# Performance work log

Measured on AMD Instinct MI355X. Metric: run time of the kernel, lower is better.

## Reference

```python
import jax, jax.numpy as jnp
import numpy as np

IN_DIM, OUT_DIM = 64, 64
HIDDEN = [64, 64, 64]
D = IN_DIM * OUT_DIM  # number of independent per-edge small MLPs
B = 256


def setup_inputs() -> dict:
    key = jax.random.key(0)
    ks = jax.random.split(key, 10)

    def kaiming(k, shape, fan_in):
        # kaiming_uniform_ with a=0, nonlinearity='relu': bound = sqrt(6/fan_in)
        bound = np.sqrt(6.0 / fan_in)
        return jax.random.uniform(k, shape, jnp.float32, -bound, bound)

    def bias_init(k, shape, fan_in):
        bound = 1.0 / np.sqrt(fan_in)
        return jax.random.uniform(k, shape, jnp.float32, -bound, bound)

    h0, h1, h2 = HIDDEN
    inp = {
        "x": jax.random.normal(ks[0], (B, IN_DIM), jnp.float32),
        # Input_Linear: weight (out_dim, in_dim, h0); fan_in per torch kaiming on this tensor is in_dim*h0,
        # bias uses reset_parameters(1) -> fan_in=1
        "w0": kaiming(ks[1], (OUT_DIM, IN_DIM, h0), IN_DIM * h0),
        "b0": bias_init(ks[2], (D, h0), 1),
        # Linear(d, o=h1, i=h0): weight (d, h1, h0); kaiming fan_in = h0 (last dim), bias fan_in = i = h0
        "w1": kaiming(ks[3], (D, h1, h0), h0),
        "b1": bias_init(ks[4], (D, h1), h0),
        "w2": kaiming(ks[5], (D, h2, h1), h1),
        "b2": bias_init(ks[6], (D, h2), h1),
        # Output_Linear: weight (out_dim, in_dim*h2), fan_in = in_dim*h2
        "wout": kaiming(ks[7], (OUT_DIM, IN_DIM * h2), IN_DIM * h2),
        "bout": bias_init(ks[8], (OUT_DIM,), IN_DIM * h2),
    }
    return inp


def reference(x, w0, b0, w1, b1, w2, b2, wout, bout):
    Bsz = x.shape[0]
    # Input_Linear: broadcast outer product -> (B, out_dim, in_dim, h0) -> (B, d, h0)
    out = x[:, None, :, None] * w0[None, :, :, :]
    out = out.reshape(Bsz, D, HIDDEN[0]) + b0[None, :, :]
    out = jax.nn.relu(out)
    # Hidden per-edge Linear layers: 'doi,Bdi->Bdo'
    out = jnp.einsum('doi,bdi->bdo', w1, out) + b1[None, :, :]
    out = jax.nn.relu(out)
    out = jnp.einsum('doi,bdi->bdo', w2, out) + b2[None, :, :]
    out = jax.nn.relu(out)
    # Output_Linear: (B, d, h2) -> (B, out_dim, in_dim*h2); 'oi,boi->bo'
    xv = out.reshape(Bsz, OUT_DIM, IN_DIM * HIDDEN[-1])
    return jnp.einsum('oi,boi->bo', wout, xv) + bout[None, :]
```

## Files before the change

### kernel.cpp

```cpp
#include <hip/hip_runtime.h>
#include <hip/hip_bf16.h>


#define D_EDGES 4096

typedef __attribute__((ext_vector_type(4))) float f32x4;
typedef __attribute__((ext_vector_type(8))) short bf16x8;

__device__ __forceinline__ unsigned pk2(float a, float b) {
    __hip_bfloat162 h = __float22bfloat162_rn(float2{a, b});
    return *reinterpret_cast<unsigned*>(&h);
}

__device__ __forceinline__ bf16x8 mk8(unsigned a, unsigned b, unsigned c, unsigned d) {
    uint4 u{a, b, c, d};
    return __builtin_bit_cast(bf16x8, u);
}

__device__ __forceinline__ int rho(int n) {
    return (n & 0x23) | ((n & 0x18) >> 1) | ((n & 0x04) << 2);
}

__global__ __launch_bounds__(256, 3) void kan_mfma(
    const float* __restrict__ x,
    const float* __restrict__ w0g,
    const float* __restrict__ b0g,
    const float* __restrict__ w1g,
    const float* __restrict__ b1g,
    const float* __restrict__ w2g,
    const float* __restrict__ b2g,
    const float* __restrict__ woutg,
    float* __restrict__ outbuf,
    int atomic_mode)
{
    const int d = blockIdx.x, o = d >> 6, ii = d & 63;
    const int t = threadIdx.x;
    const int lane = t & 63, wv = t >> 6;

    __shared__ __align__(16) unsigned char W1s[64 * 128];
    __shared__ __align__(16) unsigned char W2s[64 * 128];
    __shared__ __align__(16) float sx[256];
    __shared__ __align__(16) float sw0[64], sb0[64], sb1[64], sb2[64], swo[64];

    {
        const int orow = t >> 2, q = t & 3;
        const int prow = rho(orow);
        const unsigned swz1  = (unsigned)((prow & 7) << 4);
        const unsigned base1 = (unsigned)(prow * 128);
        const unsigned swz2  = (unsigned)((orow & 7) << 4);
        const unsigned base2 = (unsigned)(orow * 128);
        const float* s1 = w1g + (size_t)d * 4096 + orow * 64 + q * 16;
        const float* s2 = w2g + (size_t)d * 4096 + orow * 64 + q * 16;

        float4 a0 = ((const float4*)s1)[0], a1 = ((const float4*)s1)[1];
        float4 a2 = ((const float4*)s1)[2], a3 = ((const float4*)s1)[3];
        uint4 u0 = { pk2(a0.x, a0.y), pk2(a0.z, a0.w), pk2(a1.x, a1.y), pk2(a1.z, a1.w) };
        uint4 u1 = { pk2(a2.x, a2.y), pk2(a2.z, a2.w), pk2(a3.x, a3.y), pk2(a3.z, a3.w) };
        *(uint4*)&W1s[base1 + ((unsigned)(q * 32)      ^ swz1)] = u0;
        *(uint4*)&W1s[base1 + ((unsigned)(q * 32 + 16) ^ swz1)] = u1;

        a0 = ((const float4*)s2)[0]; a1 = ((const float4*)s2)[1];
        a2 = ((const float4*)s2)[2]; a3 = ((const float4*)s2)[3];
        uint4 v0 = { pk2(a0.x, a0.y), pk2(a0.z, a0.w), pk2(a1.x, a1.y), pk2(a1.z, a1.w) };
        uint4 v1 = { pk2(a2.x, a2.y), pk2(a2.z, a2.w), pk2(a3.x, a3.y), pk2(a3.z, a3.w) };
        *(uint4*)&W2s[base2 + ((unsigned)(q * 32)      ^ swz2)] = v0;
        *(uint4*)&W2s[base2 + ((unsigned)(q * 32 + 16) ^ swz2)] = v1;
    }
    sx[t] = x[t * 64 + ii];
    if (t < 64) {
        sw0[t] = w0g[(size_t)d * 64 + t];
        sb0[t] = b0g[(size_t)d * 64 + t];
        sb1[t] = b1g[(size_t)d * 64 + t];
        sb2[t] = b2g[(size_t)d * 64 + t];
        swo[t] = woutg[(size_t)o * 4096 + ii * 64 + t];
    }
    __syncthreads();

    const int arow = lane & 15;
    const int kb   = (lane >> 4) * 16;
    const int g8   = (lane >> 4) * 8;
    const unsigned lswz = (unsigned)((lane & 7) << 4);
    const int r0 = (lane >> 4) * 4;

    bf16x8 wf1[4][2], wf2[4][2];
#pragma unroll
    for (int nt = 0; nt < 4; ++nt)
#pragma unroll
        for (int ks = 0; ks < 2; ++ks) {
            wf1[nt][ks] = *(const bf16x8*)&W1s[(nt * 16 + arow) * 128 +
                            ((unsigned)(ks * 64 + kb) ^ lswz)];
            wf2[nt][ks] = *(const bf16x8*)&W2s[(nt * 16 + arow) * 128 +
                            ((unsigned)(ks * 64 + kb) ^ lswz)];
        }

    float4 w0v[2][2], b0v[2][2];
#pragma unroll
    for (int ks = 0; ks < 2; ++ks) {
        const int k0 = ks * 32 + g8;
        w0v[ks][0] = *(const float4*)&sw0[k0];
        w0v[ks][1] = *(const float4*)&sw0[k0 + 4];
        b0v[ks][0] = *(const float4*)&sb0[k0];
        b0v[ks][1] = *(const float4*)&sb0[k0 + 4];
    }

    f32x4 b1h[4], b2h[4];
    float4 woh[4];
#pragma unroll
    for (int nt = 0; nt < 4; ++nt) {
        const int bb_ = ((nt >> 1) << 5) + ((nt & 1) << 2) + g8;
        b1h[nt] = *(const f32x4*)&sb1[bb_];
        b2h[nt] = *(const f32x4*)&sb2[nt * 16 + r0];
        woh[nt] = *(const float4*)&swo[nt * 16 + r0];
    }
    float xms[4];
#pragma unroll
    for (int mti = 0; mti < 4; ++mti)
        xms[mti] = sx[wv * 64 + mti * 16 + arow];

#pragma unroll
    for (int mti = 0; mti < 4; ++mti) {
        const float xm = xms[mti];

        f32x4 a1[4] = { b1h[0], b1h[1], b1h[2], b1h[3] };
#pragma unroll
        for (int ks = 0; ks < 2; ++ks) {
            float4 wa = w0v[ks][0], wb = w0v[ks][1];
            float4 ba = b0v[ks][0], bb = b0v[ks][1];
            float v0 = fmaxf(fmaf(xm, wa.x, ba.x), 0.f);
            float v1 = fmaxf(fmaf(xm, wa.y, ba.y), 0.f);
            float v2 = fmaxf(fmaf(xm, wa.z, ba.z), 0.f);
            float v3 = fmaxf(fmaf(xm, wa.w, ba.w), 0.f);
            float v4 = fmaxf(fmaf(xm, wb.x, bb.x), 0.f);
            float v5 = fmaxf(fmaf(xm, wb.y, bb.y), 0.f);
            float v6 = fmaxf(fmaf(xm, wb.z, bb.z), 0.f);
            float v7 = fmaxf(fmaf(xm, wb.w, bb.w), 0.f);
            bf16x8 bh = mk8(pk2(v0, v1), pk2(v2, v3), pk2(v4, v5), pk2(v6, v7));
#pragma unroll
            for (int nt = 0; nt < 4; ++nt)
                a1[nt] = __builtin_amdgcn_mfma_f32_16x16x32_bf16(
                    wf1[nt][ks], bh, a1[nt], 0, 0, 0);
        }

        unsigned l0 = pk2(fmaxf(a1[0][0], 0.f), fmaxf(a1[0][1], 0.f));
        unsigned h0 = pk2(fmaxf(a1[0][2], 0.f), fmaxf(a1[0][3], 0.f));
        unsigned l1 = pk2(fmaxf(a1[1][0], 0.f), fmaxf(a1[1][1], 0.f));
        unsigned h1 = pk2(fmaxf(a1[1][2], 0.f), fmaxf(a1[1][3], 0.f));
        unsigned l2 = pk2(fmaxf(a1[2][0], 0.f), fmaxf(a1[2][1], 0.f));
        unsigned h2 = pk2(fmaxf(a1[2][2], 0.f), fmaxf(a1[2][3], 0.f));
        unsigned l3 = pk2(fmaxf(a1[3][0], 0.f), fmaxf(a1[3][1], 0.f));
        unsigned h3 = pk2(fmaxf(a1[3][2], 0.f), fmaxf(a1[3][3], 0.f));
        bf16x8 f0 = mk8(l0, h0, l1, h1);
        bf16x8 f1 = mk8(l2, h2, l3, h3);

        f32x4 a2[4] = { b2h[0], b2h[1], b2h[2], b2h[3] };
#pragma unroll
        for (int nt = 0; nt < 4; ++nt) {
            a2[nt] = __builtin_amdgcn_mfma_f32_16x16x32_bf16(
                wf2[nt][0], f0, a2[nt], 0, 0, 0);
            a2[nt] = __builtin_amdgcn_mfma_f32_16x16x32_bf16(
                wf2[nt][1], f1, a2[nt], 0, 0, 0);
        }

        float p0 = fmaxf(a2[0][0], 0.f) * woh[0].x;
        p0 = fmaf(fmaxf(a2[0][1], 0.f), woh[0].y, p0);
        p0 = fmaf(fmaxf(a2[0][2], 0.f), woh[0].z, p0);
        p0 = fmaf(fmaxf(a2[0][3], 0.f), woh[0].w, p0);
        float p1 = fmaxf(a2[1][0], 0.f) * woh[1].x;
        p1 = fmaf(fmaxf(a2[1][1], 0.f), woh[1].y, p1);
        p1 = fmaf(fmaxf(a2[1][2], 0.f), woh[1].z, p1);
        p1 = fmaf(fmaxf(a2[1][3], 0.f), woh[1].w, p1);
        float p2 = fmaxf(a2[2][0], 0.f) * woh[2].x;
        p2 = fmaf(fmaxf(a2[2][1], 0.f), woh[2].y, p2);
        p2 = fmaf(fmaxf(a2[2][2], 0.f), woh[2].z, p2);
        p2 = fmaf(fmaxf(a2[2][3], 0.f), woh[2].w, p2);
        float p3 = fmaxf(a2[3][0], 0.f) * woh[3].x;
        p3 = fmaf(fmaxf(a2[3][1], 0.f), woh[3].y, p3);
        p3 = fmaf(fmaxf(a2[3][2], 0.f), woh[3].z, p3);
        p3 = fmaf(fmaxf(a2[3][3], 0.f), woh[3].w, p3);
        float p = (p0 + p1) + (p2 + p3);

        p += __shfl_xor(p, 16);
        p += __shfl_xor(p, 32);
        const int b = wv * 64 + mti * 16 + arow;
        if (lane < 16) {
            if (atomic_mode) atomicAdd(&outbuf[b * 64 + o], p);
            else             outbuf[(size_t)d * 256 + b] = p;
        }
    }
}

__global__ __launch_bounds__(64) void kan_reduce(
    const float* __restrict__ partial,
    const float* __restrict__ bout,
    float* __restrict__ y)
{
    const int o  = blockIdx.x;
    const int b  = blockIdx.y * 64 + threadIdx.x;
    float acc = bout[o];
    const float* p = partial + (size_t)o * (64 * 256) + b;
#pragma unroll
    for (int i = 0; i < 64; ++i)
        acc += p[i * 256];
    y[b * 64 + o] = acc;
}

__global__ __launch_bounds__(256) void kan_init_out(const float* __restrict__ bout,
                                                    float* __restrict__ y)
{
    const int idx = blockIdx.x * 256 + threadIdx.x;
    y[idx] = bout[idx & 63];
}

extern "C" void kernel_launch(void* const* d_in, const int* in_sizes, int n_in,
                              void* d_out, int out_size, void* d_ws, size_t ws_size,
                              hipStream_t stream) {
    const float* x    = (const float*)d_in[0];
    const float* w0   = (const float*)d_in[1];
    const float* b0   = (const float*)d_in[2];
    const float* w1   = (const float*)d_in[3];
    const float* b1   = (const float*)d_in[4];
    const float* w2   = (const float*)d_in[5];
    const float* b2   = (const float*)d_in[6];
    const float* wout = (const float*)d_in[7];
    const float* bout = (const float*)d_in[8];
    float* y = (float*)d_out;

    const size_t partial_bytes = (size_t)D_EDGES * 256 * sizeof(float);

    if (ws_size >= partial_bytes) {
        float* partial = (float*)d_ws;
        kan_mfma<<<D_EDGES, 256, 0, stream>>>(x, w0, b0, w1, b1, w2, b2, wout, partial, 0);
        kan_reduce<<<dim3(64, 4), 64, 0, stream>>>(partial, bout, y);
    } else {
        kan_init_out<<<64, 256, 0, stream>>>(bout, y);
        kan_mfma<<<D_EDGES, 256, 0, stream>>>(x, w0, b0, w1, b1, w2, b2, wout, y, 1);
    }
}
```

Baseline: 44.86 us.

## Compute output projection with MFMA and permute W2 rows to chain layers in registers

Stores W2 rows with the same rho permutation as W1 so layer-2 accumulators come out in the layout needed as a B-operand. The final output-linear dot product then runs as two MFMAs against a masked wout A-operand (only row 0 nonzero), replacing the scalar FMA chain and cross-lane shuffles. Biases are reloaded from LDS per iteration to cut register pressure, and launch bounds go up to 4 blocks per CU. In exchange the layer-2 activations are rounded to bf16 before the output projection, and the output MFMAs use only one of their sixteen rows.

```diff
diff --git a/kernel.cpp b/kernel.cpp
--- a/kernel.cpp
+++ b/kernel.cpp
@@ -21,7 +21,7 @@
     return (n & 0x23) | ((n & 0x18) >> 1) | ((n & 0x04) << 2);
 }
 
-__global__ __launch_bounds__(256, 3) void kan_mfma(
+__global__ __launch_bounds__(256, 4) void kan_mfma(
     const float* __restrict__ x,
     const float* __restrict__ w0g,
     const float* __restrict__ b0g,
@@ -45,10 +45,8 @@
     {
         const int orow = t >> 2, q = t & 3;
         const int prow = rho(orow);
-        const unsigned swz1  = (unsigned)((prow & 7) << 4);
-        const unsigned base1 = (unsigned)(prow * 128);
-        const unsigned swz2  = (unsigned)((orow & 7) << 4);
-        const unsigned base2 = (unsigned)(orow * 128);
+        const unsigned swz  = (unsigned)((prow & 7) << 4);
+        const unsigned base = (unsigned)(prow * 128);
         const float* s1 = w1g + (size_t)d * 4096 + orow * 64 + q * 16;
         const float* s2 = w2g + (size_t)d * 4096 + orow * 64 + q * 16;
 
@@ -56,15 +54,15 @@
         float4 a2 = ((const float4*)s1)[2], a3 = ((const float4*)s1)[3];
         uint4 u0 = { pk2(a0.x, a0.y), pk2(a0.z, a0.w), pk2(a1.x, a1.y), pk2(a1.z, a1.w) };
         uint4 u1 = { pk2(a2.x, a2.y), pk2(a2.z, a2.w), pk2(a3.x, a3.y), pk2(a3.z, a3.w) };
-        *(uint4*)&W1s[base1 + ((unsigned)(q * 32)      ^ swz1)] = u0;
-        *(uint4*)&W1s[base1 + ((unsigned)(q * 32 + 16) ^ swz1)] = u1;
+        *(uint4*)&W1s[base + ((unsigned)(q * 32)      ^ swz)] = u0;
+        *(uint4*)&W1s[base + ((unsigned)(q * 32 + 16) ^ swz)] = u1;
 
         a0 = ((const float4*)s2)[0]; a1 = ((const float4*)s2)[1];
         a2 = ((const float4*)s2)[2]; a3 = ((const float4*)s2)[3];
         uint4 v0 = { pk2(a0.x, a0.y), pk2(a0.z, a0.w), pk2(a1.x, a1.y), pk2(a1.z, a1.w) };
         uint4 v1 = { pk2(a2.x, a2.y), pk2(a2.z, a2.w), pk2(a3.x, a3.y), pk2(a3.z, a3.w) };
-        *(uint4*)&W2s[base2 + ((unsigned)(q * 32)      ^ swz2)] = v0;
-        *(uint4*)&W2s[base2 + ((unsigned)(q * 32 + 16) ^ swz2)] = v1;
+        *(uint4*)&W2s[base + ((unsigned)(q * 32)      ^ swz)] = v0;
+        *(uint4*)&W2s[base + ((unsigned)(q * 32 + 16) ^ swz)] = v1;
     }
     sx[t] = x[t * 64 + ii];
     if (t < 64) {
@@ -80,7 +78,7 @@
     const int kb   = (lane >> 4) * 16;
     const int g8   = (lane >> 4) * 8;
     const unsigned lswz = (unsigned)((lane & 7) << 4);
-    const int r0 = (lane >> 4) * 4;
+    const f32x4 zero4 = { 0.f, 0.f, 0.f, 0.f };
 
     bf16x8 wf1[4][2], wf2[4][2];
 #pragma unroll
@@ -102,26 +100,34 @@
         b0v[ks][0] = *(const float4*)&sb0[k0];
         b0v[ks][1] = *(const float4*)&sb0[k0 + 4];
     }
-
-    f32x4 b1h[4], b2h[4];
-    float4 woh[4];
-#pragma unroll
-    for (int nt = 0; nt < 4; ++nt) {
-        const int bb_ = ((nt >> 1) << 5) + ((nt & 1) << 2) + g8;
-        b1h[nt] = *(const f32x4*)&sb1[bb_];
-        b2h[nt] = *(const f32x4*)&sb2[nt * 16 + r0];
-        woh[nt] = *(const float4*)&swo[nt * 16 + r0];
-    }
     float xms[4];
 #pragma unroll
     for (int mti = 0; mti < 4; ++mti)
         xms[mti] = sx[wv * 64 + mti * 16 + arow];
 
+    bf16x8 woA[2];
+#pragma unroll
+    for (int ks = 0; ks < 2; ++ks) {
+        const int k0 = ks * 32 + g8;
+        float4 wa = *(const float4*)&swo[k0];
+        float4 wb = *(const float4*)&swo[k0 + 4];
+        unsigned u0 = pk2(wa.x, wa.y), u1 = pk2(wa.z, wa.w);
+        unsigned u2 = pk2(wb.x, wb.y), u3 = pk2(wb.z, wb.w);
+        const bool keep = (arow == 0);
+        woA[ks] = mk8(keep ? u0 : 0u, keep ? u1 : 0u,
+                      keep ? u2 : 0u, keep ? u3 : 0u);
+    }
+
 #pragma unroll
     for (int mti = 0; mti < 4; ++mti) {
         const float xm = xms[mti];
 
-        f32x4 a1[4] = { b1h[0], b1h[1], b1h[2], b1h[3] };
+        f32x4 a1[4];
+#pragma unroll
+        for (int nt = 0; nt < 4; ++nt) {
+            const int bb_ = ((nt >> 1) << 5) + ((nt & 1) << 2) + g8;
+            a1[nt] = *(const f32x4*)&sb1[bb_];
+        }
 #pragma unroll
         for (int ks = 0; ks < 2; ++ks) {
             float4 wa = w0v[ks][0], wb = w0v[ks][1];
@@ -141,18 +147,23 @@
                     wf1[nt][ks], bh, a1[nt], 0, 0, 0);
         }
 
-        unsigned l0 = pk2(fmaxf(a1[0][0], 0.f), fmaxf(a1[0][1], 0.f));
-        unsigned h0 = pk2(fmaxf(a1[0][2], 0.f), fmaxf(a1[0][3], 0.f));
-        unsigned l1 = pk2(fmaxf(a1[1][0], 0.f), fmaxf(a1[1][1], 0.f));
-        unsigned h1 = pk2(fmaxf(a1[1][2], 0.f), fmaxf(a1[1][3], 0.f));
-        unsigned l2 = pk2(fmaxf(a1[2][0], 0.f), fmaxf(a1[2][1], 0.f));
-        unsigned h2 = pk2(fmaxf(a1[2][2], 0.f), fmaxf(a1[2][3], 0.f));
-        unsigned l3 = pk2(fmaxf(a1[3][0], 0.f), fmaxf(a1[3][1], 0.f));
-        unsigned h3 = pk2(fmaxf(a1[3][2], 0.f), fmaxf(a1[3][3], 0.f));
-        bf16x8 f0 = mk8(l0, h0, l1, h1);
-        bf16x8 f1 = mk8(l2, h2, l3, h3);
-
-        f32x4 a2[4] = { b2h[0], b2h[1], b2h[2], b2h[3] };
+        bf16x8 f0 = mk8(
+            pk2(fmaxf(a1[0][0], 0.f), fmaxf(a1[0][1], 0.f)),
+            pk2(fmaxf(a1[0][2], 0.f), fmaxf(a1[0][3], 0.f)),
+            pk2(fmaxf(a1[1][0], 0.f), fmaxf(a1[1][1], 0.f)),
+            pk2(fmaxf(a1[1][2], 0.f), fmaxf(a1[1][3], 0.f)));
+        bf16x8 f1 = mk8(
+            pk2(fmaxf(a1[2][0], 0.f), fmaxf(a1[2][1], 0.f)),
+            pk2(fmaxf(a1[2][2], 0.f), fmaxf(a1[2][3], 0.f)),
+            pk2(fmaxf(a1[3][0], 0.f), fmaxf(a1[3][1], 0.f)),
+            pk2(fmaxf(a1[3][2], 0.f), fmaxf(a1[3][3], 0.f)));
+
+        f32x4 a2[4];
+#pragma unroll
+        for (int nt = 0; nt < 4; ++nt) {
+            const int bb_ = ((nt >> 1) << 5) + ((nt & 1) << 2) + g8;
+            a2[nt] = *(const f32x4*)&sb2[bb_];
+        }
 #pragma unroll
         for (int nt = 0; nt < 4; ++nt) {
             a2[nt] = __builtin_amdgcn_mfma_f32_16x16x32_bf16(
@@ -161,30 +172,25 @@
                 wf2[nt][1], f1, a2[nt], 0, 0, 0);
         }
 
-        float p0 = fmaxf(a2[0][0], 0.f) * woh[0].x;
-        p0 = fmaf(fmaxf(a2[0][1], 0.f), woh[0].y, p0);
-        p0 = fmaf(fmaxf(a2[0][2], 0.f), woh[0].z, p0);
-        p0 = fmaf(fmaxf(a2[0][3], 0.f), woh[0].w, p0);
-        float p1 = fmaxf(a2[1][0], 0.f) * woh[1].x;
-        p1 = fmaf(fmaxf(a2[1][1], 0.f), woh[1].y, p1);
-        p1 = fmaf(fmaxf(a2[1][2], 0.f), woh[1].z, p1);
-        p1 = fmaf(fmaxf(a2[1][3], 0.f), woh[1].w, p1);
-        float p2 = fmaxf(a2[2][0], 0.f) * woh[2].x;
-        p2 = fmaf(fmaxf(a2[2][1], 0.f), woh[2].y, p2);
-        p2 = fmaf(fmaxf(a2[2][2], 0.f), woh[2].z, p2);
-        p2 = fmaf(fmaxf(a2[2][3], 0.f), woh[2].w, p2);
-        float p3 = fmaxf(a2[3][0], 0.f) * woh[3].x;
-        p3 = fmaf(fmaxf(a2[3][1], 0.f), woh[3].y, p3);
-        p3 = fmaf(fmaxf(a2[3][2], 0.f), woh[3].z, p3);
-        p3 = fmaf(fmaxf(a2[3][3], 0.f), woh[3].w, p3);
-        float p = (p0 + p1) + (p2 + p3);
-
-        p += __shfl_xor(p, 16);
-        p += __shfl_xor(p, 32);
+        bf16x8 e0 = mk8(
+            pk2(fmaxf(a2[0][0], 0.f), fmaxf(a2[0][1], 0.f)),
+            pk2(fmaxf(a2[0][2], 0.f), fmaxf(a2[0][3], 0.f)),
+            pk2(fmaxf(a2[1][0], 0.f), fmaxf(a2[1][1], 0.f)),
+            pk2(fmaxf(a2[1][2], 0.f), fmaxf(a2[1][3], 0.f)));
+        bf16x8 e1 = mk8(
+            pk2(fmaxf(a2[2][0], 0.f), fmaxf(a2[2][1], 0.f)),
+            pk2(fmaxf(a2[2][2], 0.f), fmaxf(a2[2][3], 0.f)),
+            pk2(fmaxf(a2[3][0], 0.f), fmaxf(a2[3][1], 0.f)),
+            pk2(fmaxf(a2[3][2], 0.f), fmaxf(a2[3][3], 0.f)));
+
+        f32x4 p3 = zero4;
+        p3 = __builtin_amdgcn_mfma_f32_16x16x32_bf16(woA[0], e0, p3, 0, 0, 0);
+        p3 = __builtin_amdgcn_mfma_f32_16x16x32_bf16(woA[1], e1, p3, 0, 0, 0);
+
         const int b = wv * 64 + mti * 16 + arow;
         if (lane < 16) {
-            if (atomic_mode) atomicAdd(&outbuf[b * 64 + o], p);
-            else             outbuf[(size_t)d * 256 + b] = p;
+            if (atomic_mode) atomicAdd(&outbuf[b * 64 + o], p3[0]);
+            else             outbuf[(size_t)d * 256 + b] = p3[0];
         }
     }
 }
```

New measurement: 63.39 us. +41.3%, slower.
